# Optimization experiments

Measured on AMD Instinct MI355X. Metric: run time of the kernel, lower is better.

Reference implementation:

```python
import jax, jax.numpy as jnp
import numpy as np
from jax import lax

SIGMAS = [0.5, 1.0, 2.0, 4.0, 8.0]
FILTER_SIZE = int(4 * SIGMAS[-1] + 1)  # 33
PAD = int(2 * SIGMAS[-1])              # 16
DR = 1.0
C1 = (0.01 * DR) ** 2
C2 = (0.03 * DR) ** 2
ALPHA = 0.025
COMPENSATION = 200.0
LAMBDA_PIXEL = 100.0


def _gauss_2d(size, sigma):
    coords = np.arange(size, dtype=np.float32) - size // 2
    g = np.exp(-coords ** 2 / (2.0 * sigma ** 2))
    g = g / g.sum()
    return np.outer(g, g)  # (size, size)


def _build_g_masks():
    # Shape (15, 1, 33, 33): 3 identical copies per sigma, interleaved as in torch code.
    m = np.zeros((3 * len(SIGMAS), 1, FILTER_SIZE, FILTER_SIZE), dtype=np.float32)
    for idx, s in enumerate(SIGMAS):
        k = _gauss_2d(FILTER_SIZE, s)
        m[3 * idx + 0, 0] = k
        m[3 * idx + 1, 0] = k
        m[3 * idx + 2, 0] = k
    return jnp.asarray(m)


def _gconv(t, w):
    # Grouped conv, groups=3 (torch semantics: out channel j in group j // (O/3),
    # group g reads input channel g). 'same' padding via explicit PAD.
    return lax.conv_general_dilated(
        t, w, window_strides=(1, 1), padding=[(PAD, PAD), (PAD, PAD)],
        feature_group_count=3, dimension_numbers=('NCHW', 'OIHW', 'NCHW'))


def setup_inputs() -> dict:
    key = jax.random.key(0)
    k1, k2, k3 = jax.random.split(key, 3)
    x = jax.random.normal(k1, (8, 3, 512, 512), dtype=jnp.float32)
    y = jax.random.normal(k2, (8, 3, 512, 512), dtype=jnp.float32)
    disc_out = jax.random.normal(k3, (8, 1, 62, 62), dtype=jnp.float32)
    return {"x": x, "y": y, "disc_out": disc_out, "g_masks": _build_g_masks()}


def reference(x, y, disc_out, g_masks):
    # denormalize: tanh output [-1,1] -> [0,1]
    x = x * 0.5 + 0.5
    y = y * 0.5 + 0.5

    mux = _gconv(x, g_masks)          # (B, 15, H, W)
    muy = _gconv(y, g_masks)
    mux2 = mux * mux
    muy2 = muy * muy
    muxy = mux * muy
    sigmax2 = _gconv(x * x, g_masks) - mux2
    sigmay2 = _gconv(y * y, g_masks) - muy2
    sigmaxy = _gconv(x * y, g_masks) - muxy

    l = (2.0 * muxy + C1) / (mux2 + muy2 + C1)
    cs = (2.0 * sigmaxy + C2) / (sigmax2 + sigmay2 + C2)

    lM = l[:, -1] * l[:, -2] * l[:, -3]       # (B, H, W)
    PIcs = jnp.prod(cs, axis=1)               # (B, H, W)
    loss_ms_ssim = 1.0 - lM * PIcs

    loss_l1 = jnp.abs(x - y)                  # (B, 3, H, W)
    # narrow(0, -3, 3) -> last 3 filters (sigma=8), grouped conv then channel mean
    gaussian_l1 = _gconv(loss_l1, g_masks[-3:]).mean(axis=1)  # (B, H, W)

    loss_mix = ALPHA * loss_ms_ssim + (1.0 - ALPHA) * gaussian_l1 / DR
    loss_mix = COMPENSATION * loss_mix

    # GeneratorLoss: lambda_pixel * L1(x, y) + MSE(disc_out, 1)
    gen_loss = LAMBDA_PIXEL * jnp.mean(jnp.abs(x - y)) + jnp.mean((disc_out - 1.0) ** 2)

    return (loss_mix.mean() + gen_loss) / 2.0
```

## Files before the change

### kernel.cpp

```cpp
#include <hip/hip_runtime.h>
#include <stdint.h>


#define TILE 32
#define HALO 16
#define SSTR 72
#define PLN  (64 * SSTR)
#define PTPLN (32 * SSTR)
#define NT   256

#define C1c 1.0e-4f
#define C2c 9.0e-4f

typedef short bf16x8 __attribute__((ext_vector_type(8)));
typedef float f32x4  __attribute__((ext_vector_type(4)));
typedef unsigned short ush;

constexpr double cexp(double xx) {
  if (xx < -700.0) return 0.0;
  const double ln2 = 0.6931471805599453, il2 = 1.4426950408889634;
  double kd = xx * il2;
  long long k = (long long)(kd + (kd >= 0 ? 0.5 : -0.5));
  double r = xx - (double)k * ln2;
  double t = 1.0, s = 1.0;
  for (int i = 1; i <= 22; ++i) { t *= r / (double)i; s += t; }
  double p = 1.0, base = (k >= 0) ? 2.0 : 0.5;
  long long n = (k >= 0) ? k : -k;
  while (n) { if (n & 1) p *= base; base *= base; n >>= 1; }
  return s * p;
}
constexpr float gsi(double sigma) {
  double inv = 1.0 / (2.0 * sigma * sigma);
  double s = 0.0;
  for (int k = -16; k <= 16; ++k) s += cexp(-(double)(k * k) * inv);
  return (float)(1.0 / s);
}
constexpr float SI05 = gsi(0.5), SI10 = gsi(1.0), SI20 = gsi(2.0),
                SI40 = gsi(4.0), SI80 = gsi(8.0);

__device__ __forceinline__ unsigned f2bf_pk(float lo, float hi) {
  union { float f; unsigned u; } a, b; a.f = lo; b.f = hi;
  return __builtin_amdgcn_perm(b.u + 0x8000u, a.u + 0x8000u, 0x07060302u);
}
__device__ __forceinline__ ush f2bf1(float f) {
  union { float f; unsigned u; } c; c.f = f;
  return (ush)((c.u + 0x8000u) >> 16);
}

struct WFrag {
  bf16x8 h[2][2];
  bf16x8 v[2];
};

template<int SIG>
__device__ __forceinline__ void build_wm(ush* __restrict__ WM,
                                         const float (*__restrict__ wf5)[40],
                                         int tid, int wave, int lane,
                                         WFrag& W) {
  __syncthreads();
  #pragma unroll
  for (int i = 0; i < 8; ++i) {
    const int idx = i * 256 + tid;
    const int m = idx >> 6, k = idx & 63;
    const int t = k - m;
    const int tc = t < 0 ? 0 : (t > 32 ? 32 : t);
    float v = wf5[SIG][tc];
    v = (t >= 0 && t <= 32) ? v : 0.f;
    WM[m * SSTR + k] = f2bf1(v);
  }
  __syncthreads();
  const int l16 = lane & 15, quad = lane >> 4;
  #pragma unroll
  for (int t = 0; t < 2; ++t)
    #pragma unroll
    for (int c = 0; c < 2; ++c)
      W.h[t][c] = *(const bf16x8*)(WM + (t * 16 + l16) * SSTR + quad * 8 + 32 * c);
  const int sv0 = (wave >> 1) * 16;
  W.v[0] = *(const bf16x8*)(WM + (sv0 + l16) * SSTR + quad * 8);
  W.v[1] = *(const bf16x8*)(WM + (sv0 + l16) * SSTR + quad * 8 + 32);
}

template<int NQ>
__device__ __forceinline__ void conv_pass(const ush* __restrict__ XQ, int q0,
                                          const WFrag& W,
                                          ush* __restrict__ PT,
                                          int wave, int lane, f32x4* V) {
  const int l16 = lane & 15, quad = lane >> 4;
  const int m0 = wave * 16;
  #pragma unroll
  for (int q = 0; q < NQ; ++q) {
    const ush* xp = XQ + (q0 + q) * PLN + (m0 + l16) * SSTR + quad * 8;
    const bf16x8 a0 = *(const bf16x8*)xp;
    const bf16x8 a1 = *(const bf16x8*)(xp + 32);
    #pragma unroll
    for (int nt = 0; nt < 2; ++nt) {
      f32x4 acc = {0.f, 0.f, 0.f, 0.f};
      acc = __builtin_amdgcn_mfma_f32_16x16x32_bf16(a0, W.h[nt][0], acc, 0, 0, 0);
      acc = __builtin_amdgcn_mfma_f32_16x16x32_bf16(a1, W.h[nt][1], acc, 0, 0, 0);
      uint2 u;
      u.x = f2bf_pk(acc[0], acc[1]);
      u.y = f2bf_pk(acc[2], acc[3]);
      *(uint2*)(PT + q * PTPLN + (nt * 16 + l16) * SSTR + m0 + quad * 4) = u;
    }
  }
  __syncthreads();
  const int n0 = (wave & 1) * 16;
  #pragma unroll
  for (int q = 0; q < NQ; ++q) {
    const ush* pp = PT + q * PTPLN + (n0 + l16) * SSTR + quad * 8;
    const bf16x8 b0 = *(const bf16x8*)pp;
    const bf16x8 b1 = *(const bf16x8*)(pp + 32);
    f32x4 acc = {0.f, 0.f, 0.f, 0.f};
    acc = __builtin_amdgcn_mfma_f32_16x16x32_bf16(W.v[0], b0, acc, 0, 0, 0);
    acc = __builtin_amdgcn_mfma_f32_16x16x32_bf16(W.v[1], b1, acc, 0, 0, 0);
    V[q] = acc;
  }
}

__device__ __forceinline__ void ssim_fold(const f32x4* V, int mult, bool last,
                                          float* PIcs) {
  #pragma unroll
  for (int r = 0; r < 4; ++r) {
    const float mux = V[0][r], muy = V[1][r];
    const float A = mux * muy;
    const float Bq = mux * mux + muy * muy;
    const float S = V[2][r] + V[3][r] - Bq;
    const float sxy = V[4][r] - A;
    const float cs = (2.f * sxy + C2c) * __builtin_amdgcn_rcpf(S + C2c);
    float p = cs;
    if (mult >= 2) p *= cs;
    if (mult >= 3) p *= cs;
    if (last) {
      const float l = (2.f * A + C1c) * __builtin_amdgcn_rcpf(Bq + C1c);
      p *= l * l * l;
    }
    PIcs[r] *= p;
  }
}

__global__ __launch_bounds__(NT)
void msssim_fused_kernel(const float* __restrict__ x, const float* __restrict__ y,
                         const float* __restrict__ disc,
                         float* __restrict__ partials) {
  __shared__ ush XQ[5 * PLN];
  __shared__ ush PT[5 * PTPLN];
  __shared__ ush WM[32 * SSTR];
  __shared__ float wf5[5][40];
  __shared__ float red[12];

  const int tid = threadIdx.x;
  const int wave = tid >> 6, lane = tid & 63;
  const int bx = blockIdx.x, by = blockIdx.y, b = blockIdx.z;
  const int x0 = bx * TILE - HALO, y0 = by * TILE - HALO;
  const int blk = (b * 16 + by) * 16 + bx;

  float d2 = 0.f;
  { const int di = blk * 16 + tid;
    if (tid < 16 && di < 8 * 62 * 62) { const float dd = disc[di] - 1.f; d2 = dd * dd; } }

  if (tid < 165) {
    const int sig = tid / 33;
    const int k = tid - sig * 33;
    const float d = (float)(k - 16);
    float inv, si;
    if (sig == 0)      { inv = 2.0f;       si = SI05; }
    else if (sig == 1) { inv = 0.5f;       si = SI10; }
    else if (sig == 2) { inv = 0.125f;     si = SI20; }
    else if (sig == 3) { inv = 0.03125f;   si = SI40; }
    else               { inv = 0.0078125f; si = SI80; }
    wf5[sig][k] = __expf(-d * d * inv) * si;
  }

  const int sr = tid >> 4;
  const int sc = (tid & 15) * 4;

  float4 PX[4], PY[4];
  auto issue_loads = [&](int ch) {
    const float* __restrict__ xs = x + (size_t)(b * 3 + ch) * 262144;
    const float* __restrict__ ys = y + (size_t)(b * 3 + ch) * 262144;
    #pragma unroll
    for (int it = 0; it < 4; ++it) {
      const int r = it * 16 + sr;
      const int gy = y0 + r, gx = x0 + sc;
      const bool rowok = (gy >= 0) && (gy < 512);
      if (rowok && gx >= 0 && gx <= 508) {
        PX[it] = *(const float4*)(xs + gy * 512 + gx);
        PY[it] = *(const float4*)(ys + gy * 512 + gx);
      } else {
        float tx[4], ty[4];
        #pragma unroll
        for (int e = 0; e < 4; ++e) {
          const int g = gx + e;
          const bool ok = rowok && (g >= 0) && (g < 512);
          tx[e] = ok ? xs[gy * 512 + g] : 0.f;
          ty[e] = ok ? ys[gy * 512 + g] : 0.f;
        }
        PX[it] = make_float4(tx[0], tx[1], tx[2], tx[3]);
        PY[it] = make_float4(ty[0], ty[1], ty[2], ty[3]);
      }
    }
  };

  float PIcs[4] = {1.f, 1.f, 1.f, 1.f};
  float sad[4][4];
  #pragma unroll
  for (int it = 0; it < 4; ++it)
    #pragma unroll
    for (int e = 0; e < 4; ++e) sad[it][e] = 0.f;

  issue_loads(0);

  auto stage = [&]() {
    #pragma unroll
    for (int it = 0; it < 4; ++it) {
      const int r = it * 16 + sr;
      float xv[4] = {PX[it].x, PX[it].y, PX[it].z, PX[it].w};
      float yv[4] = {PY[it].x, PY[it].y, PY[it].z, PY[it].w};
      float q2[4], q3[4], q4[4];
      #pragma unroll
      for (int e = 0; e < 4; ++e) {
        xv[e] = fmaf(xv[e], 0.5f, 0.5f);
        yv[e] = fmaf(yv[e], 0.5f, 0.5f);
        q2[e] = xv[e] * xv[e]; q3[e] = yv[e] * yv[e];
        q4[e] = xv[e] * yv[e];
        sad[it][e] += fabsf(xv[e] - yv[e]);
      }
      const int off = r * SSTR + sc;
      *(uint2*)(XQ + 0 * PLN + off) = make_uint2(f2bf_pk(xv[0], xv[1]), f2bf_pk(xv[2], xv[3]));
      *(uint2*)(XQ + 1 * PLN + off) = make_uint2(f2bf_pk(yv[0], yv[1]), f2bf_pk(yv[2], yv[3]));
      *(uint2*)(XQ + 2 * PLN + off) = make_uint2(f2bf_pk(q2[0], q2[1]), f2bf_pk(q2[2], q2[3]));
      *(uint2*)(XQ + 3 * PLN + off) = make_uint2(f2bf_pk(q3[0], q3[1]), f2bf_pk(q3[2], q3[3]));
      *(uint2*)(XQ + 4 * PLN + off) = make_uint2(f2bf_pk(q4[0], q4[1]), f2bf_pk(q4[2], q4[3]));
    }
  };

  f32x4 V[5];
  WFrag W;

  stage();
  issue_loads(1);
  build_wm<0>(WM, wf5, tid, wave, lane, W);
  conv_pass<5>(XQ, 0, W, PT, wave, lane, V);
  ssim_fold(V, 3, false, PIcs);
  build_wm<1>(WM, wf5, tid, wave, lane, W);
  conv_pass<5>(XQ, 0, W, PT, wave, lane, V);
  ssim_fold(V, 2, false, PIcs);

  stage();
  issue_loads(2);
  __syncthreads();
  conv_pass<5>(XQ, 0, W, PT, wave, lane, V);
  ssim_fold(V, 1, false, PIcs);
  build_wm<2>(WM, wf5, tid, wave, lane, W);
  conv_pass<5>(XQ, 0, W, PT, wave, lane, V);
  ssim_fold(V, 3, false, PIcs);
  build_wm<3>(WM, wf5, tid, wave, lane, W);
  conv_pass<5>(XQ, 0, W, PT, wave, lane, V);
  ssim_fold(V, 1, false, PIcs);

  stage();
  __syncthreads();
  conv_pass<5>(XQ, 0, W, PT, wave, lane, V);
  ssim_fold(V, 2, false, PIcs);
  build_wm<4>(WM, wf5, tid, wave, lane, W);
  conv_pass<5>(XQ, 0, W, PT, wave, lane, V);
  ssim_fold(V, 3, true, PIcs);

  #pragma unroll
  for (int it = 0; it < 4; ++it) {
    const int off = (it * 16 + sr) * SSTR + sc;
    *(uint2*)(XQ + 4 * PLN + off) =
        make_uint2(f2bf_pk(sad[it][0], sad[it][1]), f2bf_pk(sad[it][2], sad[it][3]));
  }
  __syncthreads();
  f32x4 V1[1];
  conv_pass<1>(XQ, 4, W, PT, wave, lane, V1);

  float absacc = 0.f;
  if (sc >= 16 && sc < 48) {
    #pragma unroll
    for (int it = 1; it <= 2; ++it)
      #pragma unroll
      for (int e = 0; e < 4; ++e) absacc += sad[it][e];
  }

  float mixsum = 0.f;
  #pragma unroll
  for (int r = 0; r < 4; ++r) {
    const float ssim = 1.f - PIcs[r];
    mixsum += 200.f * (0.025f * ssim + 0.975f * (V1[0][r] * (1.f / 3.f)));
  }

  #pragma unroll
  for (int off = 32; off > 0; off >>= 1) {
    mixsum += __shfl_down(mixsum, off);
    absacc += __shfl_down(absacc, off);
    d2     += __shfl_down(d2, off);
  }
  if (lane == 0) { red[wave] = mixsum; red[4 + wave] = absacc; red[8 + wave] = d2; }
  __syncthreads();
  if (tid == 0) {
    float m = 0.f, a = 0.f, d = 0.f;
    #pragma unroll
    for (int i = 0; i < 4; ++i) { m += red[i]; a += red[4 + i]; d += red[8 + i]; }
    partials[3 * blk + 0] = m;
    partials[3 * blk + 1] = a;
    partials[3 * blk + 2] = d;
  }
}

__global__ __launch_bounds__(512)
void msssim_final_kernel(const float* __restrict__ partials,
                         float* __restrict__ out) {
  __shared__ float red[24];
  const int tid = threadIdx.x;
  float m = 0.f, a = 0.f, d2 = 0.f;
  for (int j = tid; j < 2048; j += 512) {
    m  += partials[3 * j + 0];
    a  += partials[3 * j + 1];
    d2 += partials[3 * j + 2];
  }
  #pragma unroll
  for (int off = 32; off > 0; off >>= 1) {
    m  += __shfl_down(m, off);
    a  += __shfl_down(a, off);
    d2 += __shfl_down(d2, off);
  }
  const int wave = tid >> 6, lane = tid & 63;
  if (lane == 0) { red[wave] = m; red[8 + wave] = a; red[16 + wave] = d2; }
  __syncthreads();
  if (tid == 0) {
    float sm = 0.f, sa = 0.f, sd = 0.f;
    #pragma unroll
    for (int i = 0; i < 8; ++i) { sm += red[i]; sa += red[8 + i]; sd += red[16 + i]; }
    const float mix_mean  = sm / (8.f * 512.f * 512.f);
    const float abs_mean  = sa / (8.f * 3.f * 512.f * 512.f);
    const float disc_mean = sd / (8.f * 62.f * 62.f);
    out[0] = 0.5f * (mix_mean + 100.f * abs_mean + disc_mean);
  }
}

extern "C" void kernel_launch(void* const* d_in, const int* in_sizes, int n_in,
                              void* d_out, int out_size, void* d_ws, size_t ws_size,
                              hipStream_t stream) {
  const float* x    = (const float*)d_in[0];
  const float* y    = (const float*)d_in[1];
  const float* disc = (const float*)d_in[2];
  float* partials = (float*)d_ws;
  dim3 grid(16, 16, 8);
  msssim_fused_kernel<<<grid, NT, 0, stream>>>(x, y, disc, partials);
  msssim_final_kernel<<<1, 512, 0, stream>>>(partials, (float*)d_out);
}
```

Measured before the change: 146.1 us.

## Stage only x and y in LDS and derive product planes in registers

The shared staging buffer now holds only the x and y planes instead of five, cutting roughly 28 KB of LDS per block. The x², y² and xy operand fragments are computed in registers from the bf16 x and y fragments. Those five fragments are loaded once per tile stage and reused across the conv passes instead of being re-read from LDS each pass, and the launch bounds now request 3 blocks per CU. The aim is higher occupancy and less LDS traffic, at the cost of more live VGPRs, possible spills, and squares computed from bf16-rounded inputs.

```diff
diff --git a/kernel.cpp b/kernel.cpp
--- a/kernel.cpp
+++ b/kernel.cpp
@@ -81,7 +81,7 @@
 }
 
 template<int NQ>
-__device__ __forceinline__ void conv_pass(const ush* __restrict__ XQ, int q0,
+__device__ __forceinline__ void conv_pass(const bf16x8 (&A)[NQ][2],
                                           const WFrag& W,
                                           ush* __restrict__ PT,
                                           int wave, int lane, f32x4* V) {
@@ -89,14 +89,11 @@
   const int m0 = wave * 16;
   #pragma unroll
   for (int q = 0; q < NQ; ++q) {
-    const ush* xp = XQ + (q0 + q) * PLN + (m0 + l16) * SSTR + quad * 8;
-    const bf16x8 a0 = *(const bf16x8*)xp;
-    const bf16x8 a1 = *(const bf16x8*)(xp + 32);
     #pragma unroll
     for (int nt = 0; nt < 2; ++nt) {
       f32x4 acc = {0.f, 0.f, 0.f, 0.f};
-      acc = __builtin_amdgcn_mfma_f32_16x16x32_bf16(a0, W.h[nt][0], acc, 0, 0, 0);
-      acc = __builtin_amdgcn_mfma_f32_16x16x32_bf16(a1, W.h[nt][1], acc, 0, 0, 0);
+      acc = __builtin_amdgcn_mfma_f32_16x16x32_bf16(A[q][0], W.h[nt][0], acc, 0, 0, 0);
+      acc = __builtin_amdgcn_mfma_f32_16x16x32_bf16(A[q][1], W.h[nt][1], acc, 0, 0, 0);
       uint2 u;
       u.x = f2bf_pk(acc[0], acc[1]);
       u.y = f2bf_pk(acc[2], acc[3]);
@@ -138,11 +135,11 @@
   }
 }
 
-__global__ __launch_bounds__(NT)
+__global__ __launch_bounds__(NT, 3)
 void msssim_fused_kernel(const float* __restrict__ x, const float* __restrict__ y,
                          const float* __restrict__ disc,
                          float* __restrict__ partials) {
-  __shared__ ush XQ[5 * PLN];
+  __shared__ ush XQ[2 * PLN];
   __shared__ ush PT[5 * PTPLN];
   __shared__ ush WM[32 * SSTR];
   __shared__ float wf5[5][40];
@@ -216,65 +213,97 @@
       const int r = it * 16 + sr;
       float xv[4] = {PX[it].x, PX[it].y, PX[it].z, PX[it].w};
       float yv[4] = {PY[it].x, PY[it].y, PY[it].z, PY[it].w};
-      float q2[4], q3[4], q4[4];
       #pragma unroll
       for (int e = 0; e < 4; ++e) {
         xv[e] = fmaf(xv[e], 0.5f, 0.5f);
         yv[e] = fmaf(yv[e], 0.5f, 0.5f);
-        q2[e] = xv[e] * xv[e]; q3[e] = yv[e] * yv[e];
-        q4[e] = xv[e] * yv[e];
         sad[it][e] += fabsf(xv[e] - yv[e]);
       }
       const int off = r * SSTR + sc;
       *(uint2*)(XQ + 0 * PLN + off) = make_uint2(f2bf_pk(xv[0], xv[1]), f2bf_pk(xv[2], xv[3]));
       *(uint2*)(XQ + 1 * PLN + off) = make_uint2(f2bf_pk(yv[0], yv[1]), f2bf_pk(yv[2], yv[3]));
-      *(uint2*)(XQ + 2 * PLN + off) = make_uint2(f2bf_pk(q2[0], q2[1]), f2bf_pk(q2[2], q2[3]));
-      *(uint2*)(XQ + 3 * PLN + off) = make_uint2(f2bf_pk(q3[0], q3[1]), f2bf_pk(q3[2], q3[3]));
-      *(uint2*)(XQ + 4 * PLN + off) = make_uint2(f2bf_pk(q4[0], q4[1]), f2bf_pk(q4[2], q4[3]));
     }
   };
 
   f32x4 V[5];
   WFrag W;
+  bf16x8 AF[5][2];
+
+  auto load_derive = [&]() {
+    const int l16 = lane & 15, quad = lane >> 4;
+    const ush* xp = XQ + (wave * 16 + l16) * SSTR + quad * 8;
+    AF[0][0] = *(const bf16x8*)xp;
+    AF[0][1] = *(const bf16x8*)(xp + 32);
+    AF[1][0] = *(const bf16x8*)(xp + PLN);
+    AF[1][1] = *(const bf16x8*)(xp + PLN + 32);
+    #pragma unroll
+    for (int c = 0; c < 2; ++c) {
+      float xf[8], yf[8];
+      #pragma unroll
+      for (int e = 0; e < 8; ++e) {
+        union { unsigned u; float f; } ax, ay;
+        ax.u = ((unsigned)(ush)AF[0][c][e]) << 16;
+        ay.u = ((unsigned)(ush)AF[1][c][e]) << 16;
+        xf[e] = ax.f; yf[e] = ay.f;
+      }
+      union { unsigned u[4]; bf16x8 v; } w2, w3, w4;
+      #pragma unroll
+      for (int p = 0; p < 4; ++p) {
+        w2.u[p] = f2bf_pk(xf[2*p] * xf[2*p], xf[2*p+1] * xf[2*p+1]);
+        w3.u[p] = f2bf_pk(yf[2*p] * yf[2*p], yf[2*p+1] * yf[2*p+1]);
+        w4.u[p] = f2bf_pk(xf[2*p] * yf[2*p], xf[2*p+1] * yf[2*p+1]);
+      }
+      AF[2][c] = w2.v; AF[3][c] = w3.v; AF[4][c] = w4.v;
+    }
+  };
 
   stage();
   issue_loads(1);
   build_wm<0>(WM, wf5, tid, wave, lane, W);
-  conv_pass<5>(XQ, 0, W, PT, wave, lane, V);
+  load_derive();
+  conv_pass<5>(AF, W, PT, wave, lane, V);
   ssim_fold(V, 3, false, PIcs);
   build_wm<1>(WM, wf5, tid, wave, lane, W);
-  conv_pass<5>(XQ, 0, W, PT, wave, lane, V);
+  conv_pass<5>(AF, W, PT, wave, lane, V);
   ssim_fold(V, 2, false, PIcs);
 
   stage();
   issue_loads(2);
   __syncthreads();
-  conv_pass<5>(XQ, 0, W, PT, wave, lane, V);
+  load_derive();
+  conv_pass<5>(AF, W, PT, wave, lane, V);
   ssim_fold(V, 1, false, PIcs);
   build_wm<2>(WM, wf5, tid, wave, lane, W);
-  conv_pass<5>(XQ, 0, W, PT, wave, lane, V);
+  conv_pass<5>(AF, W, PT, wave, lane, V);
   ssim_fold(V, 3, false, PIcs);
   build_wm<3>(WM, wf5, tid, wave, lane, W);
-  conv_pass<5>(XQ, 0, W, PT, wave, lane, V);
+  conv_pass<5>(AF, W, PT, wave, lane, V);
   ssim_fold(V, 1, false, PIcs);
 
   stage();
   __syncthreads();
-  conv_pass<5>(XQ, 0, W, PT, wave, lane, V);
+  load_derive();
+  conv_pass<5>(AF, W, PT, wave, lane, V);
   ssim_fold(V, 2, false, PIcs);
   build_wm<4>(WM, wf5, tid, wave, lane, W);
-  conv_pass<5>(XQ, 0, W, PT, wave, lane, V);
+  conv_pass<5>(AF, W, PT, wave, lane, V);
   ssim_fold(V, 3, true, PIcs);
 
   #pragma unroll
   for (int it = 0; it < 4; ++it) {
     const int off = (it * 16 + sr) * SSTR + sc;
-    *(uint2*)(XQ + 4 * PLN + off) =
+    *(uint2*)(XQ + off) =
         make_uint2(f2bf_pk(sad[it][0], sad[it][1]), f2bf_pk(sad[it][2], sad[it][3]));
   }
   __syncthreads();
+  bf16x8 SF[1][2];
+  {
+    const ush* sp = XQ + (wave * 16 + (lane & 15)) * SSTR + (lane >> 4) * 8;
+    SF[0][0] = *(const bf16x8*)sp;
+    SF[0][1] = *(const bf16x8*)(sp + 32);
+  }
   f32x4 V1[1];
-  conv_pass<1>(XQ, 4, W, PT, wave, lane, V1);
+  conv_pass<1>(SF, W, PT, wave, lane, V1);
 
   float absacc = 0.f;
   if (sc >= 16 && sc < 48) {
```

After: 184.9 us. +26.6%, slower.
